# Kernel tuning notes

Hardware: AMD Instinct MI355X
Metric: run time of the kernel (lower is better)

## Reference

```python
import jax, jax.numpy as jnp
import numpy as np

N_HEAD, D_HEAD, D_MODEL = 16, 64, 1024
BSZ, QLEN, MEMLEN = 4, 1024, 1024
KLEN = QLEN + MEMLEN
LN_EPS = 1e-5


def _rel_shift(x):
    # x: [b, q, k, n] -> Transformer-XL relative shift
    b, q, k, n = x.shape
    x = jnp.pad(x, ((0, 0), (0, 0), (1, 0), (0, 0)))  # [b, q, k+1, n]
    x = x.reshape(b, k + 1, q, n)[:, 1:]
    return x.reshape(b, q, k, n)


def _layer_norm(x, gamma, beta):
    mu = jnp.mean(x, axis=-1, keepdims=True)
    var = jnp.var(x, axis=-1, keepdims=True)
    return (x - mu) * jax.lax.rsqrt(var + LN_EPS) * gamma + beta


def setup_inputs() -> dict:
    key = jax.random.key(0)
    ks = jax.random.split(key, 8)
    w = jax.random.normal(ks[0], (BSZ, QLEN, D_MODEL), dtype=jnp.float32)
    r = jax.random.normal(ks[1], (1, KLEN, D_MODEL), dtype=jnp.float32)
    mem = jax.random.normal(ks[2], (BSZ, MEMLEN, D_MODEL), dtype=jnp.float32)
    # causal mask: key j visible iff j <= i + MEMLEN; 1 = masked
    i = jnp.arange(QLEN)[:, None]
    j = jnp.arange(KLEN)[None, :]
    attention_mask = (j > i + MEMLEN).astype(jnp.int32)
    s = 0.02
    qkv_w = jax.random.normal(ks[3], (3 * N_HEAD * D_HEAD, D_MODEL), dtype=jnp.float32) * s
    r_w = jax.random.normal(ks[4], (N_HEAD * D_HEAD, D_MODEL), dtype=jnp.float32) * s
    o_w = jax.random.normal(ks[5], (D_MODEL, N_HEAD * D_HEAD), dtype=jnp.float32) * s
    r_r_bias = jax.random.normal(ks[6], (N_HEAD, D_HEAD), dtype=jnp.float32) * s
    r_w_bias = jax.random.normal(ks[7], (N_HEAD, D_HEAD), dtype=jnp.float32) * s
    ln_gamma = jnp.ones((D_MODEL,), dtype=jnp.float32)
    ln_beta = jnp.zeros((D_MODEL,), dtype=jnp.float32)
    return {"w": w, "r": r, "mem": mem, "attention_mask": attention_mask,
            "qkv_w": qkv_w, "r_w": r_w, "o_w": o_w,
            "r_r_bias": r_r_bias, "r_w_bias": r_w_bias,
            "ln_gamma": ln_gamma, "ln_beta": ln_beta}


def reference(w, r, mem, attention_mask, qkv_w, r_w, o_w, r_r_bias, r_w_bias, ln_gamma, ln_beta):
    bsz, qlen, d_model = w.shape
    n_head, d_head = r_r_bias.shape
    scale = 1.0 / (d_head ** 0.5)
    cat = jnp.concatenate([mem, w], axis=1)                 # [b, klen, dm]
    heads = cat @ qkv_w.T                                   # post-lnorm: no pre-LN
    q, k, v = jnp.split(heads, 3, axis=-1)
    q = q[:, -qlen:]
    klen = k.shape[1]
    q = q.reshape(bsz, qlen, n_head, d_head)
    k = k.reshape(bsz, klen, n_head, d_head)
    v = v.reshape(bsz, klen, n_head, d_head)
    rk = (r @ r_w.T).reshape(-1, n_head, d_head)            # [rlen, n, d]
    AC = jnp.einsum('bind,bjnd->bijn', q + r_w_bias, k)
    BD = _rel_shift(jnp.einsum('bind,jnd->bijn', q + r_r_bias, rk))
    score = (AC + BD) * scale                               # [b, q, k, n]
    mask = (attention_mask == 1)[None, :, :, None]
    score = jnp.where(mask, -1e30, score)
    prob = jax.nn.softmax(score, axis=2)                    # softmax over keys
    vec = jnp.einsum('bijn,bjnd->bind', prob, v).reshape(bsz, qlen, n_head * d_head)
    attn_out = vec @ o_w.T
    # post layer-norm, deepnorm_alpha defaults to 1.0, dropout is identity (eval)
    return _layer_norm(w + attn_out, ln_gamma, ln_beta)
```

## Files before the change

kernel.cpp:

```cpp
#include <hip/hip_runtime.h>

typedef __attribute__((ext_vector_type(8))) __bf16 bf16x8;
typedef __attribute__((ext_vector_type(4))) __bf16 bf16x4;
typedef __attribute__((ext_vector_type(4))) float f32x4;

__device__ __forceinline__ f32x4 mfma16(bf16x8 a, bf16x8 b, f32x4 c) {
  return __builtin_amdgcn_mfma_f32_16x16x32_bf16(a, b, c, 0, 0, 0);
}

__device__ __forceinline__ void gload_lds16(const void* g, void* l) {
  __builtin_amdgcn_global_load_lds(
      (__attribute__((address_space(1))) void*)(void*)g,
      (__attribute__((address_space(3))) void*)l, 16, 0, 0);
}

__device__ __forceinline__ bf16x8 ldsfrag(const __bf16* base, int row, int lc) {
  return *(const bf16x8*)(base + row * 64 + ((lc ^ (row & 7)) << 3));
}


__global__ __launch_bounds__(256) void cast_plain(const float* __restrict__ in,
                                                  __bf16* __restrict__ out) {
  size_t t = (size_t)blockIdx.x * 256 + threadIdx.x;
  const float4* p = (const float4*)(in + t * 8);
  float4 a = p[0], b = p[1];
  bf16x8 v;
  v[0] = (__bf16)a.x; v[1] = (__bf16)a.y; v[2] = (__bf16)a.z; v[3] = (__bf16)a.w;
  v[4] = (__bf16)b.x; v[5] = (__bf16)b.y; v[6] = (__bf16)b.z; v[7] = (__bf16)b.w;
  *(bf16x8*)(out + t * 8) = v;
}

__global__ __launch_bounds__(256) void cast_cat(const float* __restrict__ mem,
                                                const float* __restrict__ w,
                                                __bf16* __restrict__ out) {
  size_t t = (size_t)blockIdx.x * 256 + threadIdx.x;
  size_t o = t * 8;
  int c = (int)(o & 1023);
  int row = (int)(o >> 10);
  int tt = row & 2047;
  int b = row >> 11;
  const float* src = (tt < 1024)
      ? (mem + ((size_t)(b * 1024 + tt) * 1024 + c))
      : (w + ((size_t)(b * 1024 + (tt - 1024)) * 1024 + c));
  float4 a = ((const float4*)src)[0], d = ((const float4*)src)[1];
  bf16x8 v;
  v[0] = (__bf16)a.x; v[1] = (__bf16)a.y; v[2] = (__bf16)a.z; v[3] = (__bf16)a.w;
  v[4] = (__bf16)d.x; v[5] = (__bf16)d.y; v[6] = (__bf16)d.z; v[7] = (__bf16)d.w;
  *(bf16x8*)(out + o) = v;
}

template <int MODE>
__global__ __launch_bounds__(256, 2) void gemm_bt(const __bf16* __restrict__ A,
                                                  const __bf16* __restrict__ B,
                                                  __bf16* __restrict__ Cb,
                                                  float* __restrict__ Cf,
                                                  const float* __restrict__ Res,
                                                  int M, int N, int K) {
  __shared__ __bf16 As[128 * 32];
  __shared__ __bf16 Bs[128 * 32];
  const int tid = threadIdx.x;
  const int wid = tid >> 6, lane = tid & 63;
  const int l15 = lane & 15, lhi = lane >> 4;
  const int wr = wid >> 1, wc = wid & 1;
  const size_t arow0 = (size_t)blockIdx.y * 128;
  const size_t brow0 = (size_t)blockIdx.x * 128;

  f32x4 acc[4][4] = {};

  const int c0 = tid, c1 = tid + 256;
  const int r0 = c0 >> 2, o0 = (c0 & 3) * 8;
  const int r1 = c1 >> 2, o1 = (c1 & 3) * 8;
  const __bf16* ga0 = A + (arow0 + r0) * K + o0;
  const __bf16* ga1 = A + (arow0 + r1) * K + o1;
  const __bf16* gb0 = B + (brow0 + r0) * K + o0;
  const __bf16* gb1 = B + (brow0 + r1) * K + o1;
  __bf16* la0 = As + wid * 512;
  __bf16* la1 = As + 2048 + wid * 512;
  __bf16* lb0 = Bs + wid * 512;
  __bf16* lb1 = Bs + 2048 + wid * 512;

  for (int k0 = 0; k0 < K; k0 += 32) {
    gload_lds16(ga0 + k0, la0);
    gload_lds16(ga1 + k0, la1);
    gload_lds16(gb0 + k0, lb0);
    gload_lds16(gb1 + k0, lb1);
    __syncthreads();
    bf16x8 af[4], bf[4];
#pragma unroll
    for (int m = 0; m < 4; ++m)
      af[m] = *(const bf16x8*)(As + (wr * 64 + m * 16 + l15) * 32 + lhi * 8);
#pragma unroll
    for (int n = 0; n < 4; ++n)
      bf[n] = *(const bf16x8*)(Bs + (wc * 64 + n * 16 + l15) * 32 + lhi * 8);
#pragma unroll
    for (int m = 0; m < 4; ++m)
#pragma unroll
      for (int n = 0; n < 4; ++n)
        acc[m][n] = mfma16(af[m], bf[n], acc[m][n]);
    __syncthreads();
  }

#pragma unroll
  for (int m = 0; m < 4; ++m)
#pragma unroll
    for (int n = 0; n < 4; ++n) {
      size_t row = arow0 + wr * 64 + m * 16 + lhi * 4;
      size_t col = brow0 + wc * 64 + n * 16 + l15;
#pragma unroll
      for (int j = 0; j < 4; ++j) {
        size_t idx = (row + j) * (size_t)N + col;
        float v = acc[m][n][j];
        if (MODE == 0) Cb[idx] = (__bf16)v;
        else Cf[idx] = v + Res[idx];
      }
    }
}

__global__ __launch_bounds__(256) void vtrans_kernel(const __bf16* __restrict__ heads,
                                                     __bf16* __restrict__ vT) {
  __shared__ __bf16 T[64][66];
  const int j0 = blockIdx.x * 64;
  const int h = blockIdx.y, b = blockIdx.z;
  const int tid = threadIdx.x;
  {
    int jj = tid >> 2, dq = tid & 3;
    const __bf16* src = heads + ((size_t)(b * 2048 + j0 + jj)) * 3072 + 2048 + h * 64 + dq * 16;
    bf16x8 a = *(const bf16x8*)src;
    bf16x8 c = *(const bf16x8*)(src + 8);
#pragma unroll
    for (int e = 0; e < 8; ++e) { T[jj][dq * 16 + e] = a[e]; T[jj][dq * 16 + 8 + e] = c[e]; }
  }
  __syncthreads();
  {
    int d = tid >> 2, jq = tid & 3;
    bf16x8 o0, o1;
#pragma unroll
    for (int e = 0; e < 8; ++e) { o0[e] = T[jq * 16 + e][d]; o1[e] = T[jq * 16 + 8 + e][d]; }
    __bf16* dst = vT + ((size_t)((b * 16 + h) * 64 + d)) * 2048 + j0 + jq * 16;
    *(bf16x8*)dst = o0;
    *(bf16x8*)(dst + 8) = o1;
  }
}

__global__ __launch_bounds__(256) void ackb_kernel(const __bf16* __restrict__ heads,
                                                   const float* __restrict__ r_w_bias,
                                                   float* __restrict__ ackb) {
  int gid = blockIdx.x * 256 + threadIdx.x;
  int j = gid & 2047, bh = gid >> 11, b = bh >> 4, h = bh & 15;
  const __bf16* kp = heads + ((size_t)(b * 2048 + j)) * 3072 + 1024 + h * 64;
  const float* bw = r_w_bias + h * 64;
  float s = 0.f;
#pragma unroll
  for (int o = 0; o < 8; ++o) {
    bf16x8 kv = *(const bf16x8*)(kp + o * 8);
#pragma unroll
    for (int e = 0; e < 8; ++e) s += (float)kv[e] * bw[o * 8 + e];
  }
  ackb[(size_t)bh * 2048 + j] = s;
}

__global__ __launch_bounds__(256) void brk_kernel(const __bf16* __restrict__ rk,
                                                  const float* __restrict__ r_r_bias,
                                                  float* __restrict__ brk) {
  int gid = blockIdx.x * 256 + threadIdx.x;
  int t = gid & 2047, h = gid >> 11;
  const __bf16* rp = rk + (size_t)t * 1024 + h * 64;
  const float* br = r_r_bias + h * 64;
  float s = 0.f;
#pragma unroll
  for (int o = 0; o < 8; ++o) {
    bf16x8 rv = *(const bf16x8*)(rp + o * 8);
#pragma unroll
    for (int e = 0; e < 8; ++e) s += (float)rv[e] * br[o * 8 + e];
  }
  brk[(size_t)h * 2048 + t] = s;
}

__global__ __launch_bounds__(256, 2) void attn_kernel(
    const __bf16* __restrict__ heads, const __bf16* __restrict__ rk,
    const __bf16* __restrict__ vT, const float* __restrict__ ackb,
    const float* __restrict__ brk, __bf16* __restrict__ vec) {
  __shared__ __bf16 Ks[64 * 64];
  __shared__ __bf16 Vt[64 * 64];
  __shared__ __bf16 BP[4 * 2 * 16 * 88];

  int lin = blockIdx.x + (blockIdx.y << 3) + (blockIdx.z << 7);
  int nid = ((lin & 7) << 6) + (lin >> 3);
  const int bq = nid & 7, h = (nid >> 3) & 15, b = nid >> 7;

  const int tid = threadIdx.x;
  const int wid = tid >> 6, lane = tid & 63;
  const int l15 = lane & 15, lhi = lane >> 4;
  const int i0 = bq * 128 + wid * 32;

  bf16x8 q[2][2];
#pragma unroll
  for (int m = 0; m < 2; ++m) {
    const __bf16* qp =
        heads + ((size_t)(b * 2048 + 1024 + i0 + m * 16 + l15)) * 3072 + h * 64 + lhi * 8;
    q[m][0] = *(const bf16x8*)qp;
    q[m][1] = *(const bf16x8*)(qp + 32);
  }

  const float* ackbp = ackb + ((size_t)(b * 16 + h)) * 2048;
  const float* brkp = brk + (size_t)h * 2048;

  float m_run[2][4], l_run[2][4];
  f32x4 accv[2][4];
#pragma unroll
  for (int m = 0; m < 2; ++m)
#pragma unroll
    for (int r2 = 0; r2 < 4; ++r2) {
      m_run[m][r2] = -1e30f;
      l_run[m][r2] = 0.f;
      accv[m][r2] = (f32x4){0.f, 0.f, 0.f, 0.f};
    }

  const int srow = wid * 16 + (lane >> 3);
  const int ch0 = (lane & 7) ^ (srow & 7);
  const int ch1 = (lane & 7) ^ ((srow + 8) & 7);

  const int jmax = min(2048, bq * 128 + 1152);
  for (int j0 = 0; j0 < jmax; j0 += 64) {
    __syncthreads();
    {
      const __bf16* gk0 =
          heads + ((size_t)(b * 2048 + j0 + srow)) * 3072 + 1024 + h * 64 + ch0 * 8;
      const __bf16* gk1 =
          heads + ((size_t)(b * 2048 + j0 + srow + 8)) * 3072 + 1024 + h * 64 + ch1 * 8;
      const __bf16* gv0 = vT + ((size_t)((b * 16 + h) * 64 + srow)) * 2048 + j0 + ch0 * 8;
      const __bf16* gv1 = vT + ((size_t)((b * 16 + h) * 64 + srow + 8)) * 2048 + j0 + ch1 * 8;
      gload_lds16(gk0, Ks + (wid * 16) * 64);
      gload_lds16(gk1, Ks + (wid * 16 + 8) * 64);
      gload_lds16(gv0, Vt + (wid * 16) * 64);
      gload_lds16(gv1, Vt + (wid * 16 + 8) * 64);
    }
    __syncthreads();
    if (j0 > i0 + 1055) continue;

    f32x4 s[2][4];
#pragma unroll
    for (int jt = 0; jt < 4; ++jt) {
      float ai = ackbp[j0 + jt * 16 + l15];
      f32x4 init = {ai, ai, ai, ai};
      bf16x8 k0 = ldsfrag(Ks, jt * 16 + l15, lhi);
      bf16x8 k1 = ldsfrag(Ks, jt * 16 + l15, 4 + lhi);
#pragma unroll
      for (int m = 0; m < 2; ++m)
        s[m][jt] = mfma16(q[m][1], k1, mfma16(q[m][0], k0, init));
    }

#pragma unroll
    for (int m = 0; m < 2; ++m) {
      __bf16* bandm = BP + ((wid * 2 + m) * 16) * 88;
      const int tbase = j0 + 1008 - i0 - m * 16;
#pragma unroll
      for (int ct = 0; ct < 5; ++ct) {
        int trow = min(tbase + ct * 16 + l15, 2047);
        const __bf16* rp = rk + (size_t)trow * 1024 + h * 64 + lhi * 8;
        bf16x8 r0 = *(const bf16x8*)rp;
        bf16x8 r1 = *(const bf16x8*)(rp + 32);
        int cb = ct * 16 + lhi * 4;
        f32x4 init = {brkp[min(tbase + cb, 2047)], brkp[min(tbase + cb + 1, 2047)],
                      brkp[min(tbase + cb + 2, 2047)], brkp[min(tbase + cb + 3, 2047)]};
        f32x4 bd = mfma16(r1, q[m][1], mfma16(r0, q[m][0], init));
        bf16x4 bv;
        bv[0] = (__bf16)bd[0]; bv[1] = (__bf16)bd[1];
        bv[2] = (__bf16)bd[2]; bv[3] = (__bf16)bd[3];
        *(bf16x4*)(bandm + l15 * 88 + cb) = bv;
      }
    }

#pragma unroll
    for (int m = 0; m < 2; ++m) {
      __bf16* bandm = BP + ((wid * 2 + m) * 16) * 88;
#pragma unroll
      for (int jt = 0; jt < 4; ++jt) {
#pragma unroll
        for (int r2 = 0; r2 < 4; ++r2) {
          int rloc = lhi * 4 + r2;
          int jc = jt * 16 + l15;
          float v = (s[m][jt][r2] + (float)bandm[rloc * 88 + jc + 15 - rloc]) * 0.125f;
          bool msk = (j0 + jc) > (i0 + m * 16 + rloc + 1024);
          s[m][jt][r2] = msk ? -1e30f : v;
        }
      }
      float corr[4];
#pragma unroll
      for (int r2 = 0; r2 < 4; ++r2) {
        float mx = fmaxf(fmaxf(s[m][0][r2], s[m][1][r2]), fmaxf(s[m][2][r2], s[m][3][r2]));
#pragma unroll
        for (int off = 1; off < 16; off <<= 1) mx = fmaxf(mx, __shfl_xor(mx, off, 64));
        float mn = fmaxf(m_run[m][r2], mx);
        float c = __expf(m_run[m][r2] - mn);
        float rs = 0.f;
#pragma unroll
        for (int jt = 0; jt < 4; ++jt) {
          float p = __expf(s[m][jt][r2] - mn);
          s[m][jt][r2] = p;
          rs += p;
        }
#pragma unroll
        for (int off = 1; off < 16; off <<= 1) rs += __shfl_xor(rs, off, 64);
        m_run[m][r2] = mn;
        l_run[m][r2] = l_run[m][r2] * c + rs;
        corr[r2] = c;
      }
#pragma unroll
      for (int jt = 0; jt < 4; ++jt)
#pragma unroll
        for (int r2 = 0; r2 < 4; ++r2)
          bandm[(lhi * 4 + r2) * 88 + jt * 16 + l15] = (__bf16)s[m][jt][r2];
#pragma unroll
      for (int dt = 0; dt < 4; ++dt)
#pragma unroll
        for (int r2 = 0; r2 < 4; ++r2) accv[m][dt][r2] *= corr[r2];
    }

    bf16x8 ap[2][2];
#pragma unroll
    for (int m = 0; m < 2; ++m) {
      const __bf16* Pm = BP + ((wid * 2 + m) * 16) * 88;
      ap[m][0] = *(const bf16x8*)(Pm + l15 * 88 + lhi * 8);
      ap[m][1] = *(const bf16x8*)(Pm + l15 * 88 + 32 + lhi * 8);
    }
#pragma unroll
    for (int dt = 0; dt < 4; ++dt) {
      bf16x8 vf0 = ldsfrag(Vt, dt * 16 + l15, lhi);
      bf16x8 vf1 = ldsfrag(Vt, dt * 16 + l15, 4 + lhi);
#pragma unroll
      for (int m = 0; m < 2; ++m)
        accv[m][dt] = mfma16(ap[m][1], vf1, mfma16(ap[m][0], vf0, accv[m][dt]));
    }
  }

#pragma unroll
  for (int m = 0; m < 2; ++m)
#pragma unroll
    for (int dt = 0; dt < 4; ++dt)
#pragma unroll
      for (int r2 = 0; r2 < 4; ++r2) {
        int i = i0 + m * 16 + lhi * 4 + r2;
        float v = accv[m][dt][r2] / l_run[m][r2];
        vec[((size_t)(b * 1024 + i)) * 1024 + h * 64 + dt * 16 + l15] = (__bf16)v;
      }
}

__global__ __launch_bounds__(256) void ln_kernel(const float* __restrict__ pre,
                                                 const float* __restrict__ gamma,
                                                 const float* __restrict__ beta,
                                                 float* __restrict__ out) {
  const int row = blockIdx.x;
  const int tid = threadIdx.x;
  const float4 v = ((const float4*)(pre + (size_t)row * 1024))[tid];
  float s = v.x + v.y + v.z + v.w;
  float s2 = v.x * v.x + v.y * v.y + v.z * v.z + v.w * v.w;
#pragma unroll
  for (int off = 1; off < 64; off <<= 1) {
    s += __shfl_xor(s, off, 64);
    s2 += __shfl_xor(s2, off, 64);
  }
  __shared__ float red[8];
  const int wid = tid >> 6;
  if ((tid & 63) == 0) { red[wid * 2] = s; red[wid * 2 + 1] = s2; }
  __syncthreads();
  s = red[0] + red[2] + red[4] + red[6];
  s2 = red[1] + red[3] + red[5] + red[7];
  float mu = s * (1.0f / 1024.0f);
  float var = s2 * (1.0f / 1024.0f) - mu * mu;
  float rstd = rsqrtf(var + 1e-5f);
  float4 g = ((const float4*)gamma)[tid];
  float4 be = ((const float4*)beta)[tid];
  float4 o;
  o.x = (v.x - mu) * rstd * g.x + be.x;
  o.y = (v.y - mu) * rstd * g.y + be.y;
  o.z = (v.z - mu) * rstd * g.z + be.z;
  o.w = (v.w - mu) * rstd * g.w + be.w;
  ((float4*)(out + (size_t)row * 1024))[tid] = o;
}

extern "C" void kernel_launch(void* const* d_in, const int* in_sizes, int n_in,
                              void* d_out, int out_size, void* d_ws, size_t ws_size,
                              hipStream_t stream) {
  const float* w = (const float*)d_in[0];
  const float* r = (const float*)d_in[1];
  const float* mem = (const float*)d_in[2];
  const float* qkv_w = (const float*)d_in[4];
  const float* r_w = (const float*)d_in[5];
  const float* o_w = (const float*)d_in[6];
  const float* r_r_bias = (const float*)d_in[7];
  const float* r_w_bias = (const float*)d_in[8];
  const float* gamma = (const float*)d_in[9];
  const float* beta = (const float*)d_in[10];
  float* out = (float*)d_out;

  char* ws = (char*)d_ws;
  const size_t MB = 1024 * 1024;
  __bf16* catB = (__bf16*)(ws + 0);
  __bf16* vT = (__bf16*)(ws + 0);
  float* pre = (float*)(ws + 0);
  __bf16* qkvwB = (__bf16*)(ws + 16 * MB);
  __bf16* rB = (__bf16*)(ws + 22 * MB);
  __bf16* rwB = (__bf16*)(ws + 26 * MB);
  __bf16* owB = (__bf16*)(ws + 28 * MB);
  __bf16* headsB = (__bf16*)(ws + 30 * MB);
  __bf16* rkB = (__bf16*)(ws + 78 * MB);
  __bf16* vecB = (__bf16*)(ws + 82 * MB);
  float* ackbF = (float*)(ws + 90 * MB);
  float* brkF = (float*)(ws + 91 * MB);

  cast_cat<<<4096, 256, 0, stream>>>(mem, w, catB);
  cast_plain<<<1536, 256, 0, stream>>>(qkv_w, qkvwB);
  cast_plain<<<1024, 256, 0, stream>>>(r, rB);
  cast_plain<<<512, 256, 0, stream>>>(r_w, rwB);
  cast_plain<<<512, 256, 0, stream>>>(o_w, owB);

  gemm_bt<0><<<dim3(24, 64), 256, 0, stream>>>(catB, qkvwB, headsB, nullptr, nullptr,
                                               8192, 3072, 1024);
  gemm_bt<0><<<dim3(8, 16), 256, 0, stream>>>(rB, rwB, rkB, nullptr, nullptr,
                                              2048, 1024, 1024);

  vtrans_kernel<<<dim3(32, 16, 4), 256, 0, stream>>>(headsB, vT);
  ackb_kernel<<<512, 256, 0, stream>>>(headsB, r_w_bias, ackbF);
  brk_kernel<<<128, 256, 0, stream>>>(rkB, r_r_bias, brkF);

  attn_kernel<<<dim3(8, 16, 4), 256, 0, stream>>>(headsB, rkB, vT, ackbF, brkF, vecB);

  gemm_bt<1><<<dim3(8, 32), 256, 0, stream>>>(vecB, owB, nullptr, pre, w,
                                              4096, 1024, 1024);
  ln_kernel<<<4096, 256, 0, stream>>>(pre, gamma, beta, out);
}
```

Before: 355.9 us.

## Restructure attention into 64-row blocks with LDS ring buffer for relative keys

The attention kernel now uses 64-query-row blocks, with one 16-row tile per wave, and 1024 blocks scheduled longest-first. Relative-position key rows are staged through a 128-row LDS ring buffer loaded asynchronously, replacing per-lane global loads. The 1/sqrt(d) scale is folded into q and the bias vectors, and brk is padded so loads need no clamping. The operands are also transposed so softmax reductions need fewer shuffles. In exchange, occupancy is raised to 3 blocks per CU, K/V tiles are loaded twice as many times overall, and scaling q before the bf16 cast changes rounding slightly.

Result: faster. 298.3 us (-16.2%).

```diff
diff --git a/kernel.cpp b/kernel.cpp
--- a/kernel.cpp
+++ b/kernel.cpp
@@ -156,194 +156,197 @@
 #pragma unroll
     for (int e = 0; e < 8; ++e) s += (float)kv[e] * bw[o * 8 + e];
   }
-  ackb[(size_t)bh * 2048 + j] = s;
+  ackb[(size_t)bh * 2048 + j] = s * 0.125f;
 }
 
 __global__ __launch_bounds__(256) void brk_kernel(const __bf16* __restrict__ rk,
                                                   const float* __restrict__ r_r_bias,
                                                   float* __restrict__ brk) {
   int gid = blockIdx.x * 256 + threadIdx.x;
-  int t = gid & 2047, h = gid >> 11;
-  const __bf16* rp = rk + (size_t)t * 1024 + h * 64;
-  const float* br = r_r_bias + h * 64;
+  int t = gid % 2304, h = gid / 2304;
   float s = 0.f;
-#pragma unroll
-  for (int o = 0; o < 8; ++o) {
-    bf16x8 rv = *(const bf16x8*)(rp + o * 8);
-#pragma unroll
-    for (int e = 0; e < 8; ++e) s += (float)rv[e] * br[o * 8 + e];
-  }
-  brk[(size_t)h * 2048 + t] = s;
-}
-
-__global__ __launch_bounds__(256, 2) void attn_kernel(
+  if (t < 2048) {
+    const __bf16* rp = rk + (size_t)t * 1024 + h * 64;
+    const float* br = r_r_bias + h * 64;
+#pragma unroll
+    for (int o = 0; o < 8; ++o) {
+      bf16x8 rv = *(const bf16x8*)(rp + o * 8);
+#pragma unroll
+      for (int e = 0; e < 8; ++e) s += (float)rv[e] * br[o * 8 + e];
+    }
+  }
+  brk[(size_t)h * 2304 + t] = s * 0.125f;
+}
+
+__global__ __launch_bounds__(256, 3) void attn_kernel(
     const __bf16* __restrict__ heads, const __bf16* __restrict__ rk,
     const __bf16* __restrict__ vT, const float* __restrict__ ackb,
     const float* __restrict__ brk, __bf16* __restrict__ vec) {
   __shared__ __bf16 Ks[64 * 64];
   __shared__ __bf16 Vt[64 * 64];
-  __shared__ __bf16 BP[4 * 2 * 16 * 88];
-
-  int lin = blockIdx.x + (blockIdx.y << 3) + (blockIdx.z << 7);
-  int nid = ((lin & 7) << 6) + (lin >> 3);
-  const int bq = nid & 7, h = (nid >> 3) & 15, b = nid >> 7;
+  __shared__ __bf16 Ring[128 * 64];
+  __shared__ __bf16 BPa[4][16 * 88];
+
+  const int lin = blockIdx.x;
+  const int seq = lin >> 3;
+  const int bq = 15 - (seq >> 3);
+  const int rem = seq & 7;
+  const int b = rem >> 1;
+  const int h = (lin & 7) + ((rem & 1) << 3);
+  const int base = bq << 6;
 
   const int tid = threadIdx.x;
   const int wid = tid >> 6, lane = tid & 63;
   const int l15 = lane & 15, lhi = lane >> 4;
-  const int i0 = bq * 128 + wid * 32;
-
-  bf16x8 q[2][2];
-#pragma unroll
-  for (int m = 0; m < 2; ++m) {
+  const int i0 = base + wid * 16;
+
+  const int srow8 = lane >> 3;
+  const int sch = (lane & 7) ^ (srow8 & 7);
+
+  bf16x8 q0, q1;
+  {
     const __bf16* qp =
-        heads + ((size_t)(b * 2048 + 1024 + i0 + m * 16 + l15)) * 3072 + h * 64 + lhi * 8;
-    q[m][0] = *(const bf16x8*)qp;
-    q[m][1] = *(const bf16x8*)(qp + 32);
+        heads + ((size_t)(b * 2048 + 1024 + i0 + l15)) * 3072 + h * 64 + lhi * 8;
+    bf16x8 a = *(const bf16x8*)qp;
+    bf16x8 c = *(const bf16x8*)(qp + 32);
+#pragma unroll
+    for (int e = 0; e < 8; ++e) {
+      q0[e] = (__bf16)((float)a[e] * 0.125f);
+      q1[e] = (__bf16)((float)c[e] * 0.125f);
+    }
   }
 
   const float* ackbp = ackb + ((size_t)(b * 16 + h)) * 2048;
-  const float* brkp = brk + (size_t)h * 2048;
-
-  float m_run[2][4], l_run[2][4];
-  f32x4 accv[2][4];
-#pragma unroll
-  for (int m = 0; m < 2; ++m)
-#pragma unroll
-    for (int r2 = 0; r2 < 4; ++r2) {
-      m_run[m][r2] = -1e30f;
-      l_run[m][r2] = 0.f;
-      accv[m][r2] = (f32x4){0.f, 0.f, 0.f, 0.f};
-    }
-
-  const int srow = wid * 16 + (lane >> 3);
-  const int ch0 = (lane & 7) ^ (srow & 7);
-  const int ch1 = (lane & 7) ^ ((srow + 8) & 7);
-
-  const int jmax = min(2048, bq * 128 + 1152);
-  for (int j0 = 0; j0 < jmax; j0 += 64) {
+  const float* brkp = brk + (size_t)h * 2304;
+  __bf16* BP = BPa[wid];
+
+  float m_run = -1e30f, l_run = 0.f;
+  f32x4 accv[4] = {};
+
+  {
+    int r0 = 960 - base + wid * 16 + srow8;
+    gload_lds16(rk + (size_t)r0 * 1024 + h * 64 + sch * 8,
+                Ring + (((960 - base) + wid * 16) & 127) * 64);
+    gload_lds16(rk + (size_t)(r0 + 8) * 1024 + h * 64 + sch * 8,
+                Ring + (((960 - base) + wid * 16 + 8) & 127) * 64);
+  }
+
+  const int jmaxb = min(2048, base + 1088);
+  for (int j0 = 0; j0 < jmaxb; j0 += 64) {
     __syncthreads();
     {
-      const __bf16* gk0 =
-          heads + ((size_t)(b * 2048 + j0 + srow)) * 3072 + 1024 + h * 64 + ch0 * 8;
-      const __bf16* gk1 =
-          heads + ((size_t)(b * 2048 + j0 + srow + 8)) * 3072 + 1024 + h * 64 + ch1 * 8;
-      const __bf16* gv0 = vT + ((size_t)((b * 16 + h) * 64 + srow)) * 2048 + j0 + ch0 * 8;
-      const __bf16* gv1 = vT + ((size_t)((b * 16 + h) * 64 + srow + 8)) * 2048 + j0 + ch1 * 8;
-      gload_lds16(gk0, Ks + (wid * 16) * 64);
-      gload_lds16(gk1, Ks + (wid * 16 + 8) * 64);
-      gload_lds16(gv0, Vt + (wid * 16) * 64);
-      gload_lds16(gv1, Vt + (wid * 16 + 8) * 64);
+      const __bf16* kst =
+          heads + ((size_t)(b * 2048 + j0 + wid * 16 + srow8)) * 3072 + 1024 + h * 64 + sch * 8;
+      gload_lds16(kst, Ks + wid * 16 * 64);
+      gload_lds16(kst + (size_t)8 * 3072, Ks + (wid * 16 + 8) * 64);
+      const __bf16* vst =
+          vT + ((size_t)((b * 16 + h) * 64 + wid * 16 + srow8)) * 2048 + j0 + sch * 8;
+      gload_lds16(vst, Vt + wid * 16 * 64);
+      gload_lds16(vst + (size_t)8 * 2048, Vt + (wid * 16 + 8) * 64);
+      int T0 = j0 + 1024 - base;
+      int rr = T0 + wid * 16 + srow8;
+      gload_lds16(rk + (size_t)min(rr, 2047) * 1024 + h * 64 + sch * 8,
+                  Ring + ((T0 + wid * 16) & 127) * 64);
+      gload_lds16(rk + (size_t)min(rr + 8, 2047) * 1024 + h * 64 + sch * 8,
+                  Ring + ((T0 + wid * 16 + 8) & 127) * 64);
     }
     __syncthreads();
-    if (j0 > i0 + 1055) continue;
-
-    f32x4 s[2][4];
+    if (j0 >= i0 + 1040) continue;
+
+    const int tbase = j0 + 1008 - i0;
+
+#pragma unroll
+    for (int ct = 0; ct < 5; ++ct) {
+      int slot = (tbase + ct * 16 + l15) & 127;
+      bf16x8 a0 = ldsfrag(Ring, slot, lhi);
+      bf16x8 a1 = ldsfrag(Ring, slot, 4 + lhi);
+      f32x4 init = *(const f32x4*)(brkp + tbase + ct * 16 + lhi * 4);
+      f32x4 bd = mfma16(a1, q1, mfma16(a0, q0, init));
+      bf16x4 bv;
+      bv[0] = (__bf16)bd[0]; bv[1] = (__bf16)bd[1];
+      bv[2] = (__bf16)bd[2]; bv[3] = (__bf16)bd[3];
+      *(bf16x4*)(BP + l15 * 88 + ct * 16 + lhi * 4) = bv;
+    }
+
+    f32x4 st[4];
 #pragma unroll
     for (int jt = 0; jt < 4; ++jt) {
-      float ai = ackbp[j0 + jt * 16 + l15];
-      f32x4 init = {ai, ai, ai, ai};
       bf16x8 k0 = ldsfrag(Ks, jt * 16 + l15, lhi);
       bf16x8 k1 = ldsfrag(Ks, jt * 16 + l15, 4 + lhi);
-#pragma unroll
-      for (int m = 0; m < 2; ++m)
-        s[m][jt] = mfma16(q[m][1], k1, mfma16(q[m][0], k0, init));
-    }
-
-#pragma unroll
-    for (int m = 0; m < 2; ++m) {
-      __bf16* bandm = BP + ((wid * 2 + m) * 16) * 88;
-      const int tbase = j0 + 1008 - i0 - m * 16;
-#pragma unroll
-      for (int ct = 0; ct < 5; ++ct) {
-        int trow = min(tbase + ct * 16 + l15, 2047);
-        const __bf16* rp = rk + (size_t)trow * 1024 + h * 64 + lhi * 8;
-        bf16x8 r0 = *(const bf16x8*)rp;
-        bf16x8 r1 = *(const bf16x8*)(rp + 32);
-        int cb = ct * 16 + lhi * 4;
-        f32x4 init = {brkp[min(tbase + cb, 2047)], brkp[min(tbase + cb + 1, 2047)],
-                      brkp[min(tbase + cb + 2, 2047)], brkp[min(tbase + cb + 3, 2047)]};
-        f32x4 bd = mfma16(r1, q[m][1], mfma16(r0, q[m][0], init));
-        bf16x4 bv;
-        bv[0] = (__bf16)bd[0]; bv[1] = (__bf16)bd[1];
-        bv[2] = (__bf16)bd[2]; bv[3] = (__bf16)bd[3];
-        *(bf16x4*)(bandm + l15 * 88 + cb) = bv;
+      f32x4 init = *(const f32x4*)(ackbp + j0 + jt * 16 + lhi * 4);
+      st[jt] = mfma16(k1, q1, mfma16(k0, q0, init));
+    }
+
+    float sv[4][4];
+#pragma unroll
+    for (int jt = 0; jt < 4; ++jt)
+#pragma unroll
+      for (int r2 = 0; r2 < 4; ++r2) {
+        int jl = jt * 16 + lhi * 4 + r2;
+        float v = st[jt][r2] + (float)BP[l15 * 88 + jl + 15 - l15];
+        bool msk = (j0 + jl) > (i0 + l15 + 1024);
+        sv[jt][r2] = msk ? -1e30f : v;
       }
-    }
-
-#pragma unroll
-    for (int m = 0; m < 2; ++m) {
-      __bf16* bandm = BP + ((wid * 2 + m) * 16) * 88;
-#pragma unroll
-      for (int jt = 0; jt < 4; ++jt) {
-#pragma unroll
-        for (int r2 = 0; r2 < 4; ++r2) {
-          int rloc = lhi * 4 + r2;
-          int jc = jt * 16 + l15;
-          float v = (s[m][jt][r2] + (float)bandm[rloc * 88 + jc + 15 - rloc]) * 0.125f;
-          bool msk = (j0 + jc) > (i0 + m * 16 + rloc + 1024);
-          s[m][jt][r2] = msk ? -1e30f : v;
-        }
+
+    float mx = sv[0][0];
+#pragma unroll
+    for (int jt = 0; jt < 4; ++jt)
+#pragma unroll
+      for (int r2 = 0; r2 < 4; ++r2) mx = fmaxf(mx, sv[jt][r2]);
+    mx = fmaxf(mx, __shfl_xor(mx, 16, 64));
+    mx = fmaxf(mx, __shfl_xor(mx, 32, 64));
+    float mn = fmaxf(m_run, mx);
+    float corr = __expf(m_run - mn);
+    float rs = 0.f;
+#pragma unroll
+    for (int jt = 0; jt < 4; ++jt)
+#pragma unroll
+      for (int r2 = 0; r2 < 4; ++r2) {
+        float p = __expf(sv[jt][r2] - mn);
+        sv[jt][r2] = p;
+        rs += p;
       }
-      float corr[4];
-#pragma unroll
-      for (int r2 = 0; r2 < 4; ++r2) {
-        float mx = fmaxf(fmaxf(s[m][0][r2], s[m][1][r2]), fmaxf(s[m][2][r2], s[m][3][r2]));
-#pragma unroll
-        for (int off = 1; off < 16; off <<= 1) mx = fmaxf(mx, __shfl_xor(mx, off, 64));
-        float mn = fmaxf(m_run[m][r2], mx);
-        float c = __expf(m_run[m][r2] - mn);
-        float rs = 0.f;
-#pragma unroll
-        for (int jt = 0; jt < 4; ++jt) {
-          float p = __expf(s[m][jt][r2] - mn);
-          s[m][jt][r2] = p;
-          rs += p;
-        }
-#pragma unroll
-        for (int off = 1; off < 16; off <<= 1) rs += __shfl_xor(rs, off, 64);
-        m_run[m][r2] = mn;
-        l_run[m][r2] = l_run[m][r2] * c + rs;
-        corr[r2] = c;
-      }
-#pragma unroll
-      for (int jt = 0; jt < 4; ++jt)
-#pragma unroll
-        for (int r2 = 0; r2 < 4; ++r2)
-          bandm[(lhi * 4 + r2) * 88 + jt * 16 + l15] = (__bf16)s[m][jt][r2];
-#pragma unroll
-      for (int dt = 0; dt < 4; ++dt)
-#pragma unroll
-        for (int r2 = 0; r2 < 4; ++r2) accv[m][dt][r2] *= corr[r2];
-    }
-
-    bf16x8 ap[2][2];
-#pragma unroll
-    for (int m = 0; m < 2; ++m) {
-      const __bf16* Pm = BP + ((wid * 2 + m) * 16) * 88;
-      ap[m][0] = *(const bf16x8*)(Pm + l15 * 88 + lhi * 8);
-      ap[m][1] = *(const bf16x8*)(Pm + l15 * 88 + 32 + lhi * 8);
-    }
+    rs += __shfl_xor(rs, 16, 64);
+    rs += __shfl_xor(rs, 32, 64);
+    m_run = mn;
+    l_run = l_run * corr + rs;
+
+    float c4[4];
+#pragma unroll
+    for (int r2 = 0; r2 < 4; ++r2) c4[r2] = __shfl(corr, lhi * 4 + r2, 64);
+#pragma unroll
+    for (int dt = 0; dt < 4; ++dt)
+#pragma unroll
+      for (int r2 = 0; r2 < 4; ++r2) accv[dt][r2] *= c4[r2];
+
+#pragma unroll
+    for (int jt = 0; jt < 4; ++jt) {
+      bf16x4 pv;
+      pv[0] = (__bf16)sv[jt][0]; pv[1] = (__bf16)sv[jt][1];
+      pv[2] = (__bf16)sv[jt][2]; pv[3] = (__bf16)sv[jt][3];
+      *(bf16x4*)(BP + l15 * 88 + jt * 16 + lhi * 4) = pv;
+    }
+    bf16x8 ap0 = *(const bf16x8*)(BP + l15 * 88 + lhi * 8);
+    bf16x8 ap1 = *(const bf16x8*)(BP + l15 * 88 + 32 + lhi * 8);
 #pragma unroll
     for (int dt = 0; dt < 4; ++dt) {
       bf16x8 vf0 = ldsfrag(Vt, dt * 16 + l15, lhi);
       bf16x8 vf1 = ldsfrag(Vt, dt * 16 + l15, 4 + lhi);
-#pragma unroll
-      for (int m = 0; m < 2; ++m)
-        accv[m][dt] = mfma16(ap[m][1], vf1, mfma16(ap[m][0], vf0, accv[m][dt]));
-    }
-  }
-
-#pragma unroll
-  for (int m = 0; m < 2; ++m)
-#pragma unroll
-    for (int dt = 0; dt < 4; ++dt)
-#pragma unroll
-      for (int r2 = 0; r2 < 4; ++r2) {
-        int i = i0 + m * 16 + lhi * 4 + r2;
-        float v = accv[m][dt][r2] / l_run[m][r2];
-        vec[((size_t)(b * 1024 + i)) * 1024 + h * 64 + dt * 16 + l15] = (__bf16)v;
-      }
+      accv[dt] = mfma16(ap1, vf1, mfma16(ap0, vf0, accv[dt]));
+    }
+  }
+
+  float inv4[4];
+#pragma unroll
+  for (int r2 = 0; r2 < 4; ++r2) inv4[r2] = 1.0f / __shfl(l_run, lhi * 4 + r2, 64);
+#pragma unroll
+  for (int dt = 0; dt < 4; ++dt)
+#pragma unroll
+    for (int r2 = 0; r2 < 4; ++r2) {
+      int i = i0 + lhi * 4 + r2;
+      float v = accv[dt][r2] * inv4[r2];
+      vec[((size_t)(b * 1024 + i)) * 1024 + h * 64 + dt * 16 + l15] = (__bf16)v;
+    }
 }
 
 __global__ __launch_bounds__(256) void ln_kernel(const float* __restrict__ pre,
@@ -422,9 +425,9 @@
 
   vtrans_kernel<<<dim3(32, 16, 4), 256, 0, stream>>>(headsB, vT);
   ackb_kernel<<<512, 256, 0, stream>>>(headsB, r_w_bias, ackbF);
-  brk_kernel<<<128, 256, 0, stream>>>(rkB, r_r_bias, brkF);
-
-  attn_kernel<<<dim3(8, 16, 4), 256, 0, stream>>>(headsB, rkB, vT, ackbF, brkF, vecB);
+  brk_kernel<<<144, 256, 0, stream>>>(rkB, r_r_bias, brkF);
+
+  attn_kernel<<<1024, 256, 0, stream>>>(headsB, rkB, vT, ackbF, brkF, vecB);
 
   gemm_bt<1><<<dim3(8, 32), 256, 0, stream>>>(vecB, owB, nullptr, pre, w,
                                               4096, 1024, 1024);
```
